# Kernel optimization log

Hardware: AMD Instinct MI355X
Metric: run time of the kernel (lower is better)

The kernel has to match this reference:

```python
import jax, jax.numpy as jnp
import numpy as np

B, N, Z_DIM, H_DIM, MSG, MC = 32768, 16, 64, 128, 32, 4
HM_DIM = MSG * (1 + MC)          # 160
MLP_IN = MSG * MSG + HM_DIM      # 1184
MLP_HID = MSG * MSG              # 1024
MLP_OUT = MSG * MSG + MSG        # 1056


def _lin(k, fi, fo):
    return (jax.random.normal(k, (fi, fo), jnp.float32) / np.sqrt(fi)).astype(jnp.float32)


def setup_inputs() -> dict:
    key = jax.random.key(0)
    ks = jax.random.split(key, 16)
    return {
        "Z0": jax.random.normal(ks[0], (B, N, Z_DIM), jnp.float32),
        "h0": jax.random.normal(ks[1], (B, H_DIM), jnp.float32),
        "m_Z": jax.random.normal(ks[2], (B, N, MSG * MC), jnp.float32),
        "m_h": jax.random.normal(ks[3], (B, MSG * MC), jnp.float32),
        "W_Z1": _lin(ks[4], Z_DIM, MSG),                 # fc_Z1 (no bias)
        "W_h1": _lin(ks[5], H_DIM, MSG),                 # fc_h1
        "b_h1": jnp.zeros((MSG,), jnp.float32),
        "W_g1a": _lin(ks[6], HM_DIM, MSG),               # fc_g1[0]
        "b_g1a": jnp.zeros((MSG,), jnp.float32),
        "W_g1b": _lin(ks[7], MSG, 1),                    # fc_g1[2]
        "b_g1b": jnp.zeros((1,), jnp.float32),
        "W_Z2": _lin(ks[8], HM_DIM + 1, MSG),            # fc_Z2 (no bias)
        "W1": _lin(ks[9], MLP_IN, MLP_HID),              # BaseMLP
        "b1": jnp.zeros((MLP_HID,), jnp.float32),
        "W2": _lin(ks[10], MLP_HID, MLP_HID),
        "b2": jnp.zeros((MLP_HID,), jnp.float32),
        "W3": _lin(ks[11], MLP_HID, MLP_OUT),
        "b3": jnp.zeros((MLP_OUT,), jnp.float32),
    }


def reference(Z0, h0, m_Z, m_h, W_Z1, W_h1, b_h1, W_g1a, b_g1a, W_g1b, b_g1b,
              W_Z2, W1, b1, W2, b2, W3, b3):
    b = Z0.shape[0]
    Z = Z0 @ W_Z1                                        # [B,N,MSG]
    h = h0 @ W_h1 + b_h1                                 # [B,MSG]
    hm = jax.nn.relu(jnp.concatenate([h, m_h], axis=-1)) # [B,HM_DIM]
    gate = jax.nn.relu(hm @ W_g1a + b_g1a) @ W_g1b + b_g1b  # [B,1]
    # g = zeros_like(Z0)[...,0]; g[...,2]=1; g = g * fc_g1(hm)
    onehot2 = (jnp.arange(Z0.shape[1]) == 2).astype(Z0.dtype)  # [N]
    g = onehot2[None, :] * gate                          # [B,N]
    Zm = jnp.concatenate([Z, m_Z, g[..., None]], axis=-1) @ W_Z2  # [B,N,MSG]
    M = jnp.einsum('bni,bnj->bij', Zm, Zm).reshape(b, -1)  # [B,MSG*MSG]
    F_norm = jnp.linalg.norm(M, axis=-1, keepdims=True) + 1.0
    Mcat = jnp.concatenate([M, hm], axis=-1)             # [B,MLP_IN]
    Mout = jax.nn.relu(Mcat @ W1 + b1)
    Mout = jax.nn.relu(Mout @ W2 + b2)
    Mout = Mout @ W3 + b3                                # [B,MLP_OUT]
    Mout = Mout / F_norm
    msg = Zm.shape[-1]
    M_Zflat = Mout[..., : msg * msg].reshape(b, msg, msg)
    M_h = Mout[..., msg * msg:]                          # [B,MSG]
    M_Z = jnp.einsum('bnj,bjk->bnk', Zm, M_Zflat)        # [B,N,MSG]
    return (M_Z, M_h)
```

## Files before the change

### kernel.cpp

```cpp
#include <hip/hip_runtime.h>
#include <stdint.h>

#define N_B    32768
#define MLPOUT 1056
#define MCAT_K 1216
#define NPAD3  1280

typedef __attribute__((ext_vector_type(8)))  __bf16 bf16x8;
typedef __attribute__((ext_vector_type(4)))  float  f32x4;
typedef __attribute__((ext_vector_type(16))) float  f32x16;

__device__ __forceinline__ uint16_t f2bf(float f){
  union { float f; uint32_t u; } v; v.f = f;
  return (uint16_t)((v.u + 0x7fffu + ((v.u >> 16) & 1u)) >> 16);
}
__device__ __forceinline__ float bf2f(uint16_t h){
  union { uint32_t u; float f; } v; v.u = ((uint32_t)h) << 16; return v.f;
}
__device__ __forceinline__ void gld_lds16(const void* gp, void* lp){
  __builtin_amdgcn_global_load_lds(
    (__attribute__((address_space(1))) void*)(void*)gp,
    (__attribute__((address_space(3))) void*)lp, 16, 0, 0);
}

__global__ void transpose_cast_kernel(const float* __restrict__ in, uint16_t* __restrict__ out,
                                      int K, int N, int Kpad, int Npad)
{
  __shared__ float tile[32][33];
  const int tx = threadIdx.x & 31, ty = threadIdx.x >> 5;
  const int k0 = blockIdx.x * 32, n0 = blockIdx.y * 32;
#pragma unroll
  for (int i = 0; i < 4; i++){
    int k = k0 + ty + i*8, nn = n0 + tx;
    float v = (k < K && nn < N) ? in[(size_t)k*N + nn] : 0.0f;
    tile[ty + i*8][tx] = v;
  }
  __syncthreads();
#pragma unroll
  for (int i = 0; i < 4; i++){
    int nn = n0 + ty + i*8, k = k0 + tx;
    if (nn < Npad && k < Kpad) out[(size_t)nn*Kpad + k] = f2bf(tile[tx][ty + i*8]);
  }
}

__global__ void prep_small_kernel(const float* __restrict__ W_Z1, const float* __restrict__ W_Z2,
                                  const float* __restrict__ b3,
                                  uint16_t* __restrict__ WfH, uint16_t* __restrict__ WfL,
                                  float* __restrict__ wgG, float* __restrict__ b3p)
{
  __shared__ float wl[192*32];
  const int tid = threadIdx.x;
  for (int idx = tid; idx < 6144; idx += 256){
    int r = idx >> 5, c = idx & 31;
    float v;
    if (r < 64){
      v = 0.f;
      for (int i = 0; i < 32; i++) v += W_Z1[r*32 + i] * W_Z2[i*32 + c];
    } else v = W_Z2[(r - 32)*32 + c];
    wl[idx] = v;
  }
  __syncthreads();
  for (int q = tid; q < 768; q += 256){
    int lane = q & 63, ctkk = q >> 6;
    int ct = ctkk & 1, kk = ctkk >> 1;
    int c  = ct*16 + (lane & 15);
    int k0 = kk*32 + ((lane >> 4) << 3);
    for (int j = 0; j < 8; j++){
      float v = wl[(k0 + j)*32 + c];
      uint16_t hb = f2bf(v);
      WfH[q*8 + j] = hb;
      WfL[q*8 + j] = f2bf(v - bf2f(hb));
    }
  }
  if (tid < 32) wgG[tid] = W_Z2[160*32 + tid];
  for (int idx = tid; idx < NPAD3; idx += 256)
    b3p[idx] = (idx < MLPOUT) ? b3[idx] : 0.0f;
}

__global__ __launch_bounds__(256)
void gate_kernel(const float* __restrict__ h0, const float* __restrict__ mh,
                 const float* __restrict__ W_h1, const float* __restrict__ b_h1,
                 const float* __restrict__ W_g1a, const float* __restrict__ b_g1a,
                 const float* __restrict__ W_g1b, const float* __restrict__ b_g1b,
                 uint16_t* __restrict__ Mcat, float* __restrict__ gateOut)
{
  __shared__ float wh[128*32];
  __shared__ float wg[160*32];
  __shared__ float wgb[32], bh[32], bga[32];
  __shared__ float bgb;
  __shared__ float hrow[4][128];
  __shared__ float hms[4][160];
  const int tid = threadIdx.x, w = tid >> 6, l = tid & 63;
  for (int i = tid; i < 4096; i += 256) wh[i] = W_h1[i];
  for (int i = tid; i < 5120; i += 256) wg[i] = W_g1a[i];
  if (tid < 32){ wgb[tid] = W_g1b[tid]; bh[tid] = b_h1[tid]; bga[tid] = b_g1a[tid]; }
  if (tid == 0) bgb = b_g1b[0];
  __syncthreads();
  const int cg = l & 31, kh = l >> 5;
  for (int bi = 0; bi < 16; bi++){
    const int b = blockIdx.x*64 + w*16 + bi;
    hrow[w][l]      = h0[(size_t)b*128 + l];
    hrow[w][64 + l] = h0[(size_t)b*128 + 64 + l];
    float mh0 = mh[(size_t)b*128 + l];
    float mh1 = mh[(size_t)b*128 + 64 + l];
    float hacc = 0.f;
#pragma unroll 16
    for (int i = 0; i < 64; i++){
      int k = kh*64 + i;
      hacc += hrow[w][k] * wh[k*32 + cg];
    }
    hacc += __shfl_xor(hacc, 32);
    float hmc = fmaxf(hacc + bh[cg], 0.f);
    float r0 = fmaxf(mh0, 0.f), r1 = fmaxf(mh1, 0.f);
    if (l < 32) hms[w][l] = hmc;
    hms[w][32 + l] = r0;
    hms[w][96 + l] = r1;
    uint16_t* mc = Mcat + (size_t)b*MCAT_K + 1024;
    if (l < 32) mc[l] = f2bf(hmc);
    mc[32 + l] = f2bf(r0);
    mc[96 + l] = f2bf(r1);
    if (l < 32) mc[160 + l] = 0;
    float tacc = 0.f;
#pragma unroll 16
    for (int i = 0; i < 80; i++){
      int k = kh*80 + i;
      tacc += hms[w][k] * wg[k*32 + cg];
    }
    tacc += __shfl_xor(tacc, 32);
    float tc = fmaxf(tacc + bga[cg], 0.f);
    float gp = (l < 32) ? tc * wgb[cg] : 0.f;
#pragma unroll
    for (int s = 1; s < 64; s <<= 1) gp += __shfl_xor(gp, s);
    if (l == 0) gateOut[b] = gp + bgb;
  }
}

__global__ __launch_bounds__(256)
void zm_gram_kernel(const float* __restrict__ Z0, const float* __restrict__ mZ,
                    const uint16_t* __restrict__ WfH, const uint16_t* __restrict__ WfL,
                    const float* __restrict__ wgG, const float* __restrict__ gateB,
                    uint16_t* __restrict__ Mcat, float* __restrict__ Fn,
                    float* __restrict__ ZmOut)
{
  __shared__ __align__(16) uint16_t wfh[6144], wfl[6144];
  __shared__ float wgs[32];
  __shared__ __align__(16) uint16_t zhS[4][32*24], zlS[4][32*24];
  const int tid = threadIdx.x, w = tid >> 6, l = tid & 63;
#pragma unroll
  for (int i = 0; i < 3; i++){
    gld_lds16(WfH + (i*256 + tid)*8, &wfh[(i*256 + w*64)*8]);
    gld_lds16(WfL + (i*256 + tid)*8, &wfl[(i*256 + w*64)*8]);
  }
  if (tid < 32) wgs[tid] = wgG[tid];
  __syncthreads();
  const int n = l & 15, sl = l >> 4;
  for (int bi = 0; bi < 4; bi++){
    const int b = (blockIdx.x << 4) + (w << 2) + bi;
    bf16x8 xh[6], xl[6];
    const float* zp = Z0 + (size_t)b*1024 + n*64  + sl*8;
    const float* mp = mZ + (size_t)b*2048 + n*128 + sl*8;
#pragma unroll
    for (int kk = 0; kk < 6; kk++){
      const float* src = (kk < 2) ? (zp + kk*32) : (mp + (kk - 2)*32);
      float x[8];
      *(float4*)&x[0] = *(const float4*)src;
      *(float4*)&x[4] = *(const float4*)(src + 4);
#pragma unroll
      for (int j = 0; j < 8; j++){
        __bf16 h = (__bf16)x[j];
        xh[kk][j] = h;
        xl[kk][j] = (__bf16)(x[j] - (float)h);
      }
    }
    f32x4 za[2];
    za[0] = (f32x4)(0.f); za[1] = (f32x4)(0.f);
#pragma unroll
    for (int kk = 0; kk < 6; kk++){
#pragma unroll
      for (int ct = 0; ct < 2; ct++){
        bf16x8 whf = *(const bf16x8*)&wfh[((kk*2 + ct)*64 + l)*8];
        bf16x8 wlf = *(const bf16x8*)&wfl[((kk*2 + ct)*64 + l)*8];
        za[ct] = __builtin_amdgcn_mfma_f32_16x16x32_bf16(xh[kk], whf, za[ct], 0, 0, 0);
        za[ct] = __builtin_amdgcn_mfma_f32_16x16x32_bf16(xl[kk], whf, za[ct], 0, 0, 0);
        za[ct] = __builtin_amdgcn_mfma_f32_16x16x32_bf16(xh[kk], wlf, za[ct], 0, 0, 0);
      }
    }
    const float g = gateB[b];
    if (sl == 0){
      za[0][2] += g * wgs[n];
      za[1][2] += g * wgs[16 + n];
    }
    float* zo = ZmOut + (size_t)b*512;
#pragma unroll
    for (int ct = 0; ct < 2; ct++){
      ushort4 ph, pl;
#pragma unroll
      for (int r = 0; r < 4; r++){
        float v = za[ct][r];
        zo[(sl*4 + r)*32 + ct*16 + n] = v;
        uint16_t hb = f2bf(v);
        ((uint16_t*)&ph)[r] = hb;
        ((uint16_t*)&pl)[r] = f2bf(v - bf2f(hb));
      }
      const int c = ct*16 + n;
      *(ushort4*)&zhS[w][c*24 + sl*4] = ph;
      *(ushort4*)&zlS[w][c*24 + sl*4] = pl;
    }
    const int c2 = l & 31, n0 = (l >> 5) << 3;
    bf16x8 zhf = *(const bf16x8*)&zhS[w][c2*24 + n0];
    bf16x8 zlf = *(const bf16x8*)&zlS[w][c2*24 + n0];
    f32x16 gacc = (f32x16)(0.f);
    gacc = __builtin_amdgcn_mfma_f32_32x32x16_bf16(zhf, zhf, gacc, 0, 0, 0);
    gacc = __builtin_amdgcn_mfma_f32_32x32x16_bf16(zlf, zhf, gacc, 0, 0, 0);
    gacc = __builtin_amdgcn_mfma_f32_32x32x16_bf16(zhf, zlf, gacc, 0, 0, 0);
    float fs = 0.f;
#pragma unroll
    for (int i = 0; i < 16; i++) fs += gacc[i]*gacc[i];
#pragma unroll
    for (int s = 1; s < 64; s <<= 1) fs += __shfl_xor(fs, s);
    if (l == 0) Fn[b] = sqrtf(fs) + 1.0f;
    uint16_t* mcb = Mcat + (size_t)b*MCAT_K;
#pragma unroll
    for (int r = 0; r < 16; r++){
      int row = (r & 3) + 8*(r >> 2) + 4*(l >> 5);
      mcb[row*32 + c2] = f2bf(gacc[r]);
    }
  }
}

template<int NT, int RELU, int MODE, int NTN>
__global__ __launch_bounds__(256, 2)
void gemmq_kernel(const uint16_t* __restrict__ A, const uint16_t* __restrict__ Bt,
                  const float* __restrict__ bias, uint16_t* __restrict__ outB,
                  float* __restrict__ outF, const float* __restrict__ Fn)
{
  constexpr int KK = NT * 32;
  __shared__ __align__(16) uint16_t lds[32768];
  const int tid = threadIdx.x;
  const int w = tid >> 6, l = tid & 63;
  const int wr = w >> 1, wc = w & 1;
  const int lr = l & 15, kq = l >> 4;
  const int cs = ((kq ^ (lr & 3))) * 8;
  const int cpx = 32 * NTN;
  const int tl  = (blockIdx.x & 7) * cpx + (blockIdx.x >> 3);
  const int m0  = (tl / NTN) * 128, n0 = (tl % NTN) * 128;

  f32x4 acc[4][4];
#pragma unroll
  for (int r = 0; r < 4; r++)
#pragma unroll
    for (int c = 0; c < 4; c++) acc[r][c] = (f32x4)(0.0f);
  bf16x8 af[4], bf[4];

#define STAGE(s_, kt_) do{ \
  _Pragma("unroll") for (int j_ = 0; j_ < 2; j_++){ \
    int sl_ = j_*256 + tid; int r_ = sl_ >> 2; int c_ = (sl_ & 3) ^ (r_ & 3); \
    gld_lds16(A  + (size_t)(m0 + r_)*KK + (kt_)*32 + c_*8, \
              &lds[(s_)*8192 + (j_*256 + w*64)*8]); } \
  _Pragma("unroll") for (int j_ = 0; j_ < 2; j_++){ \
    int sl_ = j_*256 + tid; int r_ = sl_ >> 2; int c_ = (sl_ & 3) ^ (r_ & 3); \
    gld_lds16(Bt + (size_t)(n0 + r_)*KK + (kt_)*32 + c_*8, \
              &lds[(s_)*8192 + 4096 + (j_*256 + w*64)*8]); } }while(0)
#define RDFRAGS(s_) do{ \
  _Pragma("unroll") for (int r_ = 0; r_ < 4; r_++){ \
    int R_ = wr*64 + r_*16 + lr; \
    af[r_] = *(const bf16x8*)&lds[(s_)*8192 + R_*32 + cs]; } \
  _Pragma("unroll") for (int c_ = 0; c_ < 4; c_++){ \
    int R_ = wc*64 + c_*16 + lr; \
    bf[c_] = *(const bf16x8*)&lds[(s_)*8192 + 4096 + R_*32 + cs]; } }while(0)
#define DOMFMA() do{ _Pragma("unroll") for (int r_ = 0; r_ < 4; r_++) \
  _Pragma("unroll") for (int c_ = 0; c_ < 4; c_++) \
    acc[r_][c_] = __builtin_amdgcn_mfma_f32_16x16x32_bf16(af[r_], bf[c_], acc[r_][c_], 0, 0, 0); \
  }while(0)

  STAGE(0, 0); STAGE(1, 1); STAGE(2, 2);
  asm volatile("s_waitcnt vmcnt(8)" ::: "memory");
  asm volatile("s_barrier" ::: "memory");

#pragma unroll 1
  for (int t = 0; t < NT; t++){
    RDFRAGS(t & 3);
    asm volatile("s_waitcnt lgkmcnt(0)" ::: "memory");
    if (t + 2 < NT) { asm volatile("s_waitcnt vmcnt(4)" ::: "memory"); }
    else            { asm volatile("s_waitcnt vmcnt(0)" ::: "memory"); }
    asm volatile("s_barrier" ::: "memory");
    if (t + 3 < NT) STAGE((t + 3) & 3, t + 3);
    DOMFMA();
  }
#undef STAGE
#undef RDFRAGS
#undef DOMFMA

#pragma unroll
  for (int c = 0; c < 4; c++){
    const int gcol = n0 + wc*64 + c*16 + lr;
    const float bv = bias[gcol];
#pragma unroll
    for (int r = 0; r < 4; r++){
      const int grow0 = m0 + wr*64 + r*16 + kq*4;
#pragma unroll
      for (int gg = 0; gg < 4; gg++){
        float v = acc[r][c][gg] + bv;
        if (RELU) v = fmaxf(v, 0.0f);
        const int grow = grow0 + gg;
        if (MODE == 0){
          outB[(size_t)grow*1024 + gcol] = f2bf(v);
        } else {
          if (gcol < 1024)      outB[(size_t)grow*1024 + gcol] = f2bf(v);
          else if (gcol < 1056) outF[(size_t)grow*32 + (gcol - 1024)] = v / Fn[grow];
        }
      }
    }
  }
}

__global__ __launch_bounds__(256)
void epilogue_kernel(const uint16_t* __restrict__ Mzf, const float* __restrict__ Fn,
                     float* __restrict__ Out)
{
  __shared__ __align__(16) uint16_t mzS[4][1024];
  __shared__ __align__(16) float    zmS[4][16*36];
  const int tid = threadIdx.x, w = tid >> 6, l = tid & 63;
  const int n = l & 15, q = l >> 4;
  for (int bi = 0; bi < 4; bi++){
    const int b = (blockIdx.x << 4) + (w << 2) + bi;
    const uint4* src = (const uint4*)(Mzf + (size_t)b*1024);
    uint4* dst = (uint4*)&mzS[w][0];
    dst[l]      = src[l];
    dst[l + 64] = src[l + 64];
    const float4* zsrc = (const float4*)(Out + (size_t)b*512);
#pragma unroll
    for (int i = 0; i < 2; i++){
      int f = i*64 + l;
      int nn = f >> 3, c4 = f & 7;
      *(float4*)&zmS[w][nn*36 + c4*4] = zsrc[f];
    }
    float acc[8];
#pragma unroll
    for (int i = 0; i < 8; i++) acc[i] = 0.f;
#pragma unroll
    for (int j = 0; j < 32; j++){
      float zv = zmS[w][n*36 + j];
      uint4 mv = *(const uint4*)&mzS[w][j*32 + q*8];
      acc[0] += zv * bf2f((uint16_t)(mv.x & 0xffffu));
      acc[1] += zv * bf2f((uint16_t)(mv.x >> 16));
      acc[2] += zv * bf2f((uint16_t)(mv.y & 0xffffu));
      acc[3] += zv * bf2f((uint16_t)(mv.y >> 16));
      acc[4] += zv * bf2f((uint16_t)(mv.z & 0xffffu));
      acc[5] += zv * bf2f((uint16_t)(mv.z >> 16));
      acc[6] += zv * bf2f((uint16_t)(mv.w & 0xffffu));
      acc[7] += zv * bf2f((uint16_t)(mv.w >> 16));
    }
    const float inv = 1.0f / Fn[b];
    float4* op = (float4*)(Out + (size_t)b*512 + n*32 + q*8);
    op[0] = make_float4(acc[0]*inv, acc[1]*inv, acc[2]*inv, acc[3]*inv);
    op[1] = make_float4(acc[4]*inv, acc[5]*inv, acc[6]*inv, acc[7]*inv);
  }
}

extern "C" void kernel_launch(void* const* d_in, const int* in_sizes, int n_in,
                              void* d_out, int out_size, void* d_ws, size_t ws_size,
                              hipStream_t stream)
{
  const float* Z0    = (const float*)d_in[0];
  const float* h0    = (const float*)d_in[1];
  const float* mZ    = (const float*)d_in[2];
  const float* mh    = (const float*)d_in[3];
  const float* W_Z1  = (const float*)d_in[4];
  const float* W_h1  = (const float*)d_in[5];
  const float* b_h1  = (const float*)d_in[6];
  const float* W_g1a = (const float*)d_in[7];
  const float* b_g1a = (const float*)d_in[8];
  const float* W_g1b = (const float*)d_in[9];
  const float* b_g1b = (const float*)d_in[10];
  const float* W_Z2  = (const float*)d_in[11];
  const float* W1    = (const float*)d_in[12];
  const float* b1    = (const float*)d_in[13];
  const float* W2    = (const float*)d_in[14];
  const float* b2    = (const float*)d_in[15];
  const float* W3    = (const float*)d_in[16];
  const float* b3    = (const float*)d_in[17];

  char* ws = (char*)d_ws;
  size_t off = 0;
  auto alloc = [&](size_t bytes) -> char* {
    char* p = ws + off;
    off += (bytes + 255) & ~(size_t)255;
    return p;
  };
  uint16_t* W1t  = (uint16_t*)alloc((size_t)1024*MCAT_K*2);
  uint16_t* W2t  = (uint16_t*)alloc((size_t)1024*1024*2);
  uint16_t* W3t  = (uint16_t*)alloc((size_t)NPAD3*1024*2);
  float*    b3p  = (float*)   alloc((size_t)NPAD3*4);
  uint16_t* WfH  = (uint16_t*)alloc((size_t)6144*2);
  uint16_t* WfL  = (uint16_t*)alloc((size_t)6144*2);
  float*    wgG  = (float*)   alloc((size_t)32*4);
  float*    gate = (float*)   alloc((size_t)N_B*4);
  float*    Fn   = (float*)   alloc((size_t)N_B*4);
  uint16_t* Mcat = (uint16_t*)alloc((size_t)N_B*MCAT_K*2);
  uint16_t* H1   = (uint16_t*)alloc((size_t)N_B*1024*2);
  uint16_t* H2   = (uint16_t*)alloc((size_t)N_B*1024*2);
  uint16_t* Mzf  = Mcat;
  float* OutMZ = (float*)d_out;
  float* OutMH = (float*)d_out + (size_t)N_B*512;

  transpose_cast_kernel<<<dim3(38,32), 256, 0, stream>>>(W1, W1t, 1184, 1024, MCAT_K, 1024);
  transpose_cast_kernel<<<dim3(32,32), 256, 0, stream>>>(W2, W2t, 1024, 1024, 1024, 1024);
  transpose_cast_kernel<<<dim3(32,40), 256, 0, stream>>>(W3, W3t, 1024, 1056, 1024, NPAD3);
  prep_small_kernel<<<1, 256, 0, stream>>>(W_Z1, W_Z2, b3, WfH, WfL, wgG, b3p);
  gate_kernel<<<512, 256, 0, stream>>>(h0, mh, W_h1, b_h1, W_g1a, b_g1a, W_g1b, b_g1b,
                                       Mcat, gate);
  zm_gram_kernel<<<2048, 256, 0, stream>>>(Z0, mZ, WfH, WfL, wgG, gate, Mcat, Fn, OutMZ);
  gemmq_kernel<38,1,0,8><<<2048, 256, 0, stream>>>(Mcat, W1t, b1, H1, nullptr, nullptr);
  gemmq_kernel<32,1,0,8><<<2048, 256, 0, stream>>>(H1,   W2t, b2, H2, nullptr, nullptr);
  gemmq_kernel<32,0,1,9><<<2304, 256, 0, stream>>>(H2,   W3t, b3p, Mzf, OutMH, Fn);
  epilogue_kernel<<<2048, 256, 0, stream>>>(Mzf, Fn, OutMZ);
}
```

Before: 543.2 us.

## Switch MLP GEMMs to K=64 tiles with double-buffered LDS pipeline

Replaces the 4-stage K=32 LDS pipeline in the three MLP GEMMs with a 2-stage K=64 double buffer that uses an 8-way XOR swizzle. Each iteration now does twice the MFMAs per barrier, so there are half as many sync points. In exchange, prefetch depth drops to one tile ahead and each step drains vmcnt fully before its barrier, which may expose more global-load latency. Also adds an explicit vmcnt wait before the barrier in the gram kernel's weight preload.

```diff
diff --git a/kernel.cpp b/kernel.cpp
--- a/kernel.cpp
+++ b/kernel.cpp
@@ -152,6 +152,7 @@
     gld_lds16(WfL + (i*256 + tid)*8, &wfl[(i*256 + w*64)*8]);
   }
   if (tid < 32) wgs[tid] = wgG[tid];
+  asm volatile("s_waitcnt vmcnt(0)" ::: "memory");
   __syncthreads();
   const int n = l & 15, sl = l >> 4;
   for (int bi = 0; bi < 4; bi++){
@@ -230,17 +231,18 @@
 
 template<int NT, int RELU, int MODE, int NTN>
 __global__ __launch_bounds__(256, 2)
-void gemmq_kernel(const uint16_t* __restrict__ A, const uint16_t* __restrict__ Bt,
-                  const float* __restrict__ bias, uint16_t* __restrict__ outB,
-                  float* __restrict__ outF, const float* __restrict__ Fn)
-{
-  constexpr int KK = NT * 32;
+void gemmk64_kernel(const uint16_t* __restrict__ A, const uint16_t* __restrict__ Bt,
+                    const float* __restrict__ bias, uint16_t* __restrict__ outB,
+                    float* __restrict__ outF, const float* __restrict__ Fn)
+{
+  constexpr int KK = NT * 64;
   __shared__ __align__(16) uint16_t lds[32768];
   const int tid = threadIdx.x;
   const int w = tid >> 6, l = tid & 63;
   const int wr = w >> 1, wc = w & 1;
   const int lr = l & 15, kq = l >> 4;
-  const int cs = ((kq ^ (lr & 3))) * 8;
+  const int cs0 = ((kq)     ^ (lr & 7)) * 8;
+  const int cs1 = ((4 + kq) ^ (lr & 7)) * 8;
   const int cpx = 32 * NTN;
   const int tl  = (blockIdx.x & 7) * cpx + (blockIdx.x >> 3);
   const int m0  = (tl / NTN) * 128, n0 = (tl % NTN) * 128;
@@ -250,46 +252,51 @@
   for (int r = 0; r < 4; r++)
 #pragma unroll
     for (int c = 0; c < 4; c++) acc[r][c] = (f32x4)(0.0f);
-  bf16x8 af[4], bf[4];
+  bf16x8 af[4][2], bf[4][2];
 
 #define STAGE(s_, kt_) do{ \
-  _Pragma("unroll") for (int j_ = 0; j_ < 2; j_++){ \
-    int sl_ = j_*256 + tid; int r_ = sl_ >> 2; int c_ = (sl_ & 3) ^ (r_ & 3); \
-    gld_lds16(A  + (size_t)(m0 + r_)*KK + (kt_)*32 + c_*8, \
-              &lds[(s_)*8192 + (j_*256 + w*64)*8]); } \
-  _Pragma("unroll") for (int j_ = 0; j_ < 2; j_++){ \
-    int sl_ = j_*256 + tid; int r_ = sl_ >> 2; int c_ = (sl_ & 3) ^ (r_ & 3); \
-    gld_lds16(Bt + (size_t)(n0 + r_)*KK + (kt_)*32 + c_*8, \
-              &lds[(s_)*8192 + 4096 + (j_*256 + w*64)*8]); } }while(0)
+  _Pragma("unroll") for (int j_ = 0; j_ < 4; j_++){ \
+    int sl_ = j_*256 + tid; int r_ = sl_ >> 3; int c_ = (sl_ & 7) ^ (r_ & 7); \
+    gld_lds16(A  + (size_t)(m0 + r_)*KK + (kt_)*64 + c_*8, \
+              &lds[(s_)*16384 + (j_*256 + w*64)*8]); } \
+  _Pragma("unroll") for (int j_ = 0; j_ < 4; j_++){ \
+    int sl_ = j_*256 + tid; int r_ = sl_ >> 3; int c_ = (sl_ & 7) ^ (r_ & 7); \
+    gld_lds16(Bt + (size_t)(n0 + r_)*KK + (kt_)*64 + c_*8, \
+              &lds[(s_)*16384 + 8192 + (j_*256 + w*64)*8]); } }while(0)
 #define RDFRAGS(s_) do{ \
   _Pragma("unroll") for (int r_ = 0; r_ < 4; r_++){ \
-    int R_ = wr*64 + r_*16 + lr; \
-    af[r_] = *(const bf16x8*)&lds[(s_)*8192 + R_*32 + cs]; } \
+    int R_ = (wr*64 + r_*16 + lr) * 64; \
+    af[r_][0] = *(const bf16x8*)&lds[(s_)*16384 + R_ + cs0]; \
+    af[r_][1] = *(const bf16x8*)&lds[(s_)*16384 + R_ + cs1]; } \
   _Pragma("unroll") for (int c_ = 0; c_ < 4; c_++){ \
-    int R_ = wc*64 + c_*16 + lr; \
-    bf[c_] = *(const bf16x8*)&lds[(s_)*8192 + 4096 + R_*32 + cs]; } }while(0)
+    int R_ = (wc*64 + c_*16 + lr) * 64; \
+    bf[c_][0] = *(const bf16x8*)&lds[(s_)*16384 + 8192 + R_ + cs0]; \
+    bf[c_][1] = *(const bf16x8*)&lds[(s_)*16384 + 8192 + R_ + cs1]; } }while(0)
 #define DOMFMA() do{ _Pragma("unroll") for (int r_ = 0; r_ < 4; r_++) \
-  _Pragma("unroll") for (int c_ = 0; c_ < 4; c_++) \
-    acc[r_][c_] = __builtin_amdgcn_mfma_f32_16x16x32_bf16(af[r_], bf[c_], acc[r_][c_], 0, 0, 0); \
+  _Pragma("unroll") for (int c_ = 0; c_ < 4; c_++){ \
+    acc[r_][c_] = __builtin_amdgcn_mfma_f32_16x16x32_bf16(af[r_][0], bf[c_][0], acc[r_][c_], 0, 0, 0); \
+    acc[r_][c_] = __builtin_amdgcn_mfma_f32_16x16x32_bf16(af[r_][1], bf[c_][1], acc[r_][c_], 0, 0, 0); } \
   }while(0)
-
-  STAGE(0, 0); STAGE(1, 1); STAGE(2, 2);
-  asm volatile("s_waitcnt vmcnt(8)" ::: "memory");
-  asm volatile("s_barrier" ::: "memory");
+#define VMDRAIN() asm volatile("s_waitcnt vmcnt(0)" ::: "memory")
+
+  STAGE(0, 0);
+  STAGE(1, 1);
+  VMDRAIN();
+  __syncthreads();
 
 #pragma unroll 1
   for (int t = 0; t < NT; t++){
-    RDFRAGS(t & 3);
-    asm volatile("s_waitcnt lgkmcnt(0)" ::: "memory");
-    if (t + 2 < NT) { asm volatile("s_waitcnt vmcnt(4)" ::: "memory"); }
-    else            { asm volatile("s_waitcnt vmcnt(0)" ::: "memory"); }
-    asm volatile("s_barrier" ::: "memory");
-    if (t + 3 < NT) STAGE((t + 3) & 3, t + 3);
+    const int s = t & 1;
+    RDFRAGS(s);
     DOMFMA();
+    VMDRAIN();
+    __syncthreads();
+    if (t + 2 < NT) STAGE(s, t + 2);
   }
 #undef STAGE
 #undef RDFRAGS
 #undef DOMFMA
+#undef VMDRAIN
 
 #pragma unroll
   for (int c = 0; c < 4; c++){
@@ -411,8 +418,8 @@
   gate_kernel<<<512, 256, 0, stream>>>(h0, mh, W_h1, b_h1, W_g1a, b_g1a, W_g1b, b_g1b,
                                        Mcat, gate);
   zm_gram_kernel<<<2048, 256, 0, stream>>>(Z0, mZ, WfH, WfL, wgG, gate, Mcat, Fn, OutMZ);
-  gemmq_kernel<38,1,0,8><<<2048, 256, 0, stream>>>(Mcat, W1t, b1, H1, nullptr, nullptr);
-  gemmq_kernel<32,1,0,8><<<2048, 256, 0, stream>>>(H1,   W2t, b2, H2, nullptr, nullptr);
-  gemmq_kernel<32,0,1,9><<<2304, 256, 0, stream>>>(H2,   W3t, b3p, Mzf, OutMH, Fn);
+  gemmk64_kernel<19,1,0,8><<<2048, 256, 0, stream>>>(Mcat, W1t, b1, H1, nullptr, nullptr);
+  gemmk64_kernel<16,1,0,8><<<2048, 256, 0, stream>>>(H1,   W2t, b2, H2, nullptr, nullptr);
+  gemmk64_kernel<16,0,1,9><<<2304, 256, 0, stream>>>(H2,   W3t, b3p, Mzf, OutMH, Fn);
   epilogue_kernel<<<2048, 256, 0, stream>>>(Mzf, Fn, OutMZ);
 }
```

Result: faster. 531.6 us (-2.1%).
